# Kernel tuning notes

Hardware: AMD Instinct MI355X
Metric: run time of the kernel (lower is better)

Reference implementation:

```python
import jax, jax.numpy as jnp
import numpy as np

N_NODES = 100000
N_EDGES = 3200000
NUM_FEATURES = 128
NUM_CLASSES = 32
H1, H2 = 64, 32


def _glorot(key, shape):
    lim = float(np.sqrt(6.0 / (shape[0] + shape[1])))
    return jax.random.uniform(key, shape, jnp.float32, -lim, lim)


def setup_inputs() -> dict:
    key = jax.random.key(0)
    ks = jax.random.split(key, 8)
    x = jax.random.normal(ks[0], (N_NODES, NUM_FEATURES), jnp.float32)
    edge_index = jax.random.randint(ks[1], (2, N_EDGES), 0, N_NODES, jnp.int64)
    return {
        "x": x,
        "edge_index": edge_index,
        "W1": _glorot(ks[2], (NUM_FEATURES, H1)), "b1": jnp.zeros((H1,), jnp.float32),
        "W2": _glorot(ks[3], (H1, H2)), "b2": jnp.zeros((H2,), jnp.float32),
        "Wf": _glorot(ks[4], (H2, H2)), "bf": jnp.zeros((H2,), jnp.float32),
        "Wo": _glorot(ks[5], (H2, NUM_CLASSES)), "bo": jnp.zeros((NUM_CLASSES,), jnp.float32),
    }


def gcn_conv(x, src, dst, n, W, b):
    # PyG GCNConv: add self-loops, symmetric normalization D^-1/2 A D^-1/2,
    # aggregate messages source -> target (dst = edge_index[1]).
    h = x @ W                                            # [N, F_out]
    deg = jax.ops.segment_sum(jnp.ones_like(dst, dtype=x.dtype), dst, num_segments=n)
    dinv = jnp.where(deg > 0, jax.lax.rsqrt(deg), 0.0)
    norm = dinv[src] * dinv[dst]                         # [E+N]
    msg = h[src] * norm[:, None]                         # gather + scale
    return jax.ops.segment_sum(msg, dst, num_segments=n) + b


def reference(x, edge_index, W1, b1, W2, b2, Wf, bf, Wo, bo):
    n = x.shape[0]
    loops = jnp.arange(n, dtype=edge_index.dtype)
    src = jnp.concatenate([edge_index[0], loops])
    dst = jnp.concatenate([edge_index[1], loops])
    h = jax.nn.relu(gcn_conv(x, src, dst, n, W1, b1))
    h = gcn_conv(h, src, dst, n, W2, b2)
    h = jax.nn.relu(h @ Wf + bf)
    return h @ Wo + bo
```

## Files before the change

### kernel.cpp

```cpp
#include <hip/hip_runtime.h>
#include <hip/hip_bf16.h>


#define N_NODES 100000
#define N_EDGES 3200000
#define F_IN    128
#define H1F     64
#define H2F     32
#define NCLS    32
#define SCAN_BLOCK 1024
#define SCAN_CHUNKS ((N_NODES + SCAN_BLOCK - 1) / SCAN_BLOCK)
#define NTIL2 (N_NODES / 32)
#define NCNT2 ((N_EDGES + 2048 - 1) / 2048)
#define NFRONT (NTIL2 + NCNT2)

typedef __attribute__((ext_vector_type(8))) short bf16x8;
typedef __attribute__((ext_vector_type(4))) float f32x4;

static __device__ __forceinline__ float b2f(__hip_bfloat16 v) {
    return __bfloat162float(v);
}
static __device__ __forceinline__ float us2f(unsigned short u) {
    return __uint_as_float(((unsigned)u) << 16);
}
static __device__ __forceinline__ unsigned short f2us(float f) {
    __hip_bfloat16 h = __float2bfloat16(f);
    return *(unsigned short*)&h;
}
static __device__ __forceinline__ float ld(const void* p, size_t i, int isbf) {
    return isbf ? b2f(((const __hip_bfloat16*)p)[i]) : ((const float*)p)[i];
}


__global__ void k_detect(const void* xbuf, const void* eibuf, int* flags) {
    if (threadIdx.x != 0 || blockIdx.x != 0) return;
    const unsigned* ew = (const unsigned*)eibuf;
    int z = 0;
    for (int k = 0; k < 256; ++k) z += (ew[2 * k + 1] == 0u) ? 1 : 0;
    flags[0] = (z >= 200) ? 1 : 0;
    const unsigned* xw = (const unsigned*)xbuf;
    int inr = 0;
    for (int k = 0; k < 256; ++k) {
        unsigned fb = (xw[k] & 0xFFFFu) << 16;
        float a = fabsf(__uint_as_float(fb));
        inr += (a >= 1e-4f && a <= 20.0f) ? 1 : 0;
    }
    flags[1] = (inr >= 160) ? 1 : 0;
}

__global__ void __launch_bounds__(256)
k_front(const void* __restrict__ x, const void* __restrict__ W1,
        const int* __restrict__ ei,
        int* __restrict__ deg, int* __restrict__ aux,
        unsigned short* __restrict__ h1, const int* __restrict__ flags) {
    int blk = blockIdx.x, tid = threadIdx.x;

    if (blk % 3 == 0) {
        int t = (blk / 3) * 256 + tid;
        int e0 = t * 8;
        if (e0 >= N_EDGES) return;
        int d[8];
        if (flags[0]) {
            const int4* p = (const int4*)(ei + 2 * (size_t)(N_EDGES + e0));
            int4 a = p[0], b = p[1], c = p[2], g = p[3];
            d[0] = a.x; d[1] = a.z; d[2] = b.x; d[3] = b.z;
            d[4] = c.x; d[5] = c.z; d[6] = g.x; d[7] = g.z;
        } else {
            const int4* p = (const int4*)(ei + (size_t)N_EDGES + e0);
            int4 a = p[0], b = p[1];
            d[0] = a.x; d[1] = a.y; d[2] = a.z; d[3] = a.w;
            d[4] = b.x; d[5] = b.y; d[6] = b.z; d[7] = b.w;
        }
        int r[8];
#pragma unroll
        for (int j = 0; j < 8; ++j)
            r[j] = ((unsigned)d[j] < N_NODES) ? atomicAdd(&deg[d[j]], 1) : 0;
        *(int4*)(aux + e0)     = make_int4(r[0], r[1], r[2], r[3]);
        *(int4*)(aux + e0 + 4) = make_int4(r[4], r[5], r[6], r[7]);
        return;
    }

    int tile = blk - blk / 3 - 1;
    int isbf = flags[1];
    int wave = __builtin_amdgcn_readfirstlane(tid >> 6);
    int lane = tid & 63;
    size_t nbase = (size_t)tile * 32 + (size_t)wave * 8;

    float acc[8];
#pragma unroll
    for (int i = 0; i < 8; ++i) acc[i] = 0.f;

    if (isbf) {
        const unsigned short* w  = (const unsigned short*)W1;
        const unsigned short* xp = (const unsigned short*)x;
#pragma unroll 4
        for (int k2 = 0; k2 < 64; ++k2) {
            float wa = us2f(w[(2 * k2) * H1F + lane]);
            float wb = us2f(w[(2 * k2 + 1) * H1F + lane]);
#pragma unroll
            for (int i = 0; i < 8; ++i) {
                float xa = us2f(xp[(nbase + i) * F_IN + 2 * k2]);
                float xb = us2f(xp[(nbase + i) * F_IN + 2 * k2 + 1]);
                acc[i] += xa * wa;
                acc[i] += xb * wb;
            }
        }
    } else {
        const float* w  = (const float*)W1;
        const float* xp = (const float*)x;
#pragma unroll 4
        for (int k2 = 0; k2 < 64; ++k2) {
            float wa = w[(2 * k2) * H1F + lane];
            float wb = w[(2 * k2 + 1) * H1F + lane];
#pragma unroll
            for (int i = 0; i < 8; ++i) {
                float xa = xp[(nbase + i) * F_IN + 2 * k2];
                float xb = xp[(nbase + i) * F_IN + 2 * k2 + 1];
                acc[i] += xa * wa;
                acc[i] += xb * wb;
            }
        }
    }

#pragma unroll
    for (int i = 0; i < 8; ++i)
        h1[(nbase + i) * H1F + lane] = f2us(acc[i]);
}

__global__ void k_scanA(const int* __restrict__ deg, int* __restrict__ partial,
                        float* __restrict__ dinv) {
    __shared__ int red[16];
    int b = blockIdx.x, t = threadIdx.x;
    int i = b * SCAN_BLOCK + t;
    int v = (i < N_NODES) ? deg[i] : 0;
    if (i < N_NODES) dinv[i] = rsqrtf((float)v + 1.0f);
    for (int off = 32; off; off >>= 1) v += __shfl_down(v, off, 64);
    if ((t & 63) == 0) red[t >> 6] = v;
    __syncthreads();
    if (t == 0) {
        int s = 0;
        for (int k = 0; k < 16; ++k) s += red[k];
        partial[b] = s;
    }
}

__global__ void k_scanB(const int* __restrict__ partial, int* __restrict__ chunkoff) {
    if (threadIdx.x != 0 || blockIdx.x != 0) return;
    int run = 0;
    for (int b = 0; b < SCAN_CHUNKS; ++b) { chunkoff[b] = run; run += partial[b]; }
}

__global__ void k_scanC(const int* __restrict__ deg, const int* __restrict__ chunkoff,
                        int* __restrict__ rowptr) {
    __shared__ int wsum[16];
    int b = blockIdx.x, t = threadIdx.x, lane = t & 63, w = t >> 6;
    int i = b * SCAN_BLOCK + t;
    int v = (i < N_NODES) ? deg[i] : 0;
    for (int off = 1; off < 64; off <<= 1) {
        int u = __shfl_up(v, off, 64);
        if (lane >= off) v += u;
    }
    if (lane == 63) wsum[w] = v;
    __syncthreads();
    if (t == 0) {
        int run = 0;
        for (int k = 0; k < 16; ++k) { int s = wsum[k]; wsum[k] = run; run += s; }
    }
    __syncthreads();
    int incl = v + wsum[w] + chunkoff[b];
    if (i < N_NODES) rowptr[i + 1] = incl;
    if (b == 0 && t == 0) rowptr[0] = 0;
}

__global__ void __launch_bounds__(256)
k_scatter(const int* __restrict__ ei, const int* __restrict__ aux,
          const int* __restrict__ rowptr, int* __restrict__ csr,
          const int* __restrict__ flags) {
    int t = blockIdx.x * blockDim.x + threadIdx.x;
    int e0 = t * 8;
    if (e0 >= N_EDGES) return;
    int s[8], d[8];
    if (flags[0]) {
        const int4* ps = (const int4*)(ei + 2 * (size_t)e0);
#pragma unroll
        for (int q = 0; q < 4; ++q) {
            int4 a = ps[q];
            s[2 * q] = a.x; s[2 * q + 1] = a.z;
        }
        const int4* pd = (const int4*)(ei + 2 * (size_t)(N_EDGES + e0));
#pragma unroll
        for (int q = 0; q < 4; ++q) {
            int4 c = pd[q];
            d[2 * q] = c.x; d[2 * q + 1] = c.z;
        }
    } else {
        const int4* ps = (const int4*)(ei + (size_t)e0);
#pragma unroll
        for (int q = 0; q < 2; ++q) {
            int4 a = ps[q];
            s[4 * q] = a.x; s[4 * q + 1] = a.y; s[4 * q + 2] = a.z; s[4 * q + 3] = a.w;
        }
        const int4* pd = (const int4*)(ei + (size_t)N_EDGES + e0);
#pragma unroll
        for (int q = 0; q < 2; ++q) {
            int4 c = pd[q];
            d[4 * q] = c.x; d[4 * q + 1] = c.y; d[4 * q + 2] = c.z; d[4 * q + 3] = c.w;
        }
    }
    int a8[8];
    {
        int4 av0 = *(const int4*)(aux + e0);
        int4 av1 = *(const int4*)(aux + e0 + 4);
        a8[0] = av0.x; a8[1] = av0.y; a8[2] = av0.z; a8[3] = av0.w;
        a8[4] = av1.x; a8[5] = av1.y; a8[6] = av1.z; a8[7] = av1.w;
    }
    int rp[8];
#pragma unroll
    for (int j = 0; j < 8; ++j) {
        bool ok = (unsigned)s[j] < N_NODES && (unsigned)d[j] < N_NODES;
        rp[j] = ok ? rowptr[d[j]] : -1;
    }
#pragma unroll
    for (int j = 0; j < 8; ++j) {
        if (rp[j] >= 0) csr[rp[j] + a8[j]] = s[j];
    }
}

__global__ void k_agg1gemm2(const unsigned short* __restrict__ h1,
                            const float* __restrict__ dinv,
                            const int* __restrict__ rowptr, const int* __restrict__ csr,
                            const void* __restrict__ b1, const void* __restrict__ W2,
                            unsigned short* __restrict__ h2, const int* __restrict__ flags) {
    int n    = (blockIdx.x * blockDim.x + threadIdx.x) >> 6;
    n = __builtin_amdgcn_readfirstlane(n);
    int lane = threadIdx.x & 63;
    if (n >= N_NODES) return;
    int beg = rowptr[n], end = rowptr[n + 1];
    float dn  = dinv[n];
    float acc = dn * us2f(h1[(size_t)n * H1F + lane]);
    int e = beg;
    int nfull = (end - beg) >> 3;
    if (nfull > 0) {
        int sn[8];
#pragma unroll
        for (int j = 0; j < 8; ++j) sn[j] = csr[e + j];
        for (int b = 0; b < nfull; ++b) {
            int sc[8];
#pragma unroll
            for (int j = 0; j < 8; ++j) sc[j] = sn[j];
            e += 8;
            if (b + 1 < nfull) {
#pragma unroll
                for (int j = 0; j < 8; ++j) sn[j] = csr[e + j];
            }
            float w0 = dinv[sc[0]], w1 = dinv[sc[1]], w2 = dinv[sc[2]], w3 = dinv[sc[3]];
            float w4 = dinv[sc[4]], w5 = dinv[sc[5]], w6 = dinv[sc[6]], w7 = dinv[sc[7]];
            unsigned short v0 = h1[(size_t)sc[0] * H1F + lane];
            unsigned short v1 = h1[(size_t)sc[1] * H1F + lane];
            unsigned short v2 = h1[(size_t)sc[2] * H1F + lane];
            unsigned short v3 = h1[(size_t)sc[3] * H1F + lane];
            unsigned short v4 = h1[(size_t)sc[4] * H1F + lane];
            unsigned short v5 = h1[(size_t)sc[5] * H1F + lane];
            unsigned short v6 = h1[(size_t)sc[6] * H1F + lane];
            unsigned short v7 = h1[(size_t)sc[7] * H1F + lane];
            acc += w0 * us2f(v0); acc += w1 * us2f(v1);
            acc += w2 * us2f(v2); acc += w3 * us2f(v3);
            acc += w4 * us2f(v4); acc += w5 * us2f(v5);
            acc += w6 * us2f(v6); acc += w7 * us2f(v7);
        }
    }
    for (; e + 3 < end; e += 4) {
        int s0 = csr[e], s1 = csr[e + 1], s2 = csr[e + 2], s3 = csr[e + 3];
        float w0 = dinv[s0], w1 = dinv[s1], w2 = dinv[s2], w3 = dinv[s3];
        unsigned short v0 = h1[(size_t)s0 * H1F + lane];
        unsigned short v1 = h1[(size_t)s1 * H1F + lane];
        unsigned short v2 = h1[(size_t)s2 * H1F + lane];
        unsigned short v3 = h1[(size_t)s3 * H1F + lane];
        acc += w0 * us2f(v0); acc += w1 * us2f(v1);
        acc += w2 * us2f(v2); acc += w3 * us2f(v3);
    }
    for (; e < end; ++e) {
        int s = csr[e];
        acc += dinv[s] * us2f(h1[(size_t)s * H1F + lane]);
    }
    acc *= dn;
    int isbf = flags[1];
    float bv = isbf ? b2f(((const __hip_bfloat16*)b1)[lane]) : ((const float*)b1)[lane];
    float v  = fmaxf(acc + bv, 0.f);
    int f = lane & 31, h = lane >> 5;
    float part = 0.f;
    if (isbf) {
        const __hip_bfloat16* w = (const __hip_bfloat16*)W2;
#pragma unroll
        for (int j = 0; j < 32; ++j) {
            int k = h * 32 + j;
            part += __shfl(v, k, 64) * b2f(w[k * H2F + f]);
        }
    } else {
        const float* w = (const float*)W2;
#pragma unroll
        for (int j = 0; j < 32; ++j) {
            int k = h * 32 + j;
            part += __shfl(v, k, 64) * w[k * H2F + f];
        }
    }
    part += __shfl(part, lane ^ 32, 64);
    if (h == 0) h2[(size_t)n * H2F + f] = f2us(part);
}

__global__ void GCN_51737176048479_kernel(const unsigned short* __restrict__ h2,
                                          const float* __restrict__ dinv,
                                          const int* __restrict__ rowptr,
                                          const int* __restrict__ csr,
                                          const void* __restrict__ b2v,
                                          const void* __restrict__ Wf,
                                          const void* __restrict__ bfv,
                                          const void* __restrict__ Wo,
                                          const void* __restrict__ bov,
                                          void* __restrict__ out,
                                          const int* __restrict__ flags) {
    int tid = blockIdx.x * blockDim.x + threadIdx.x;
    int n   = tid >> 5;
    int f   = threadIdx.x & 31;
    if (n >= N_NODES) return;
    int isbf = flags[1];
    int beg = rowptr[n], end = rowptr[n + 1];
    float dn = dinv[n];
    float ar = dn * us2f(h2[(size_t)n * H2F + f]);
    int e = beg;
    int nfull = (end - beg) >> 3;
    if (nfull > 0) {
        int sn[8];
#pragma unroll
        for (int j = 0; j < 8; ++j) sn[j] = csr[e + j];
        for (int b = 0; b < nfull; ++b) {
            int sc[8];
#pragma unroll
            for (int j = 0; j < 8; ++j) sc[j] = sn[j];
            e += 8;
            if (b + 1 < nfull) {
#pragma unroll
                for (int j = 0; j < 8; ++j) sn[j] = csr[e + j];
            }
            float w0 = dinv[sc[0]], w1 = dinv[sc[1]], w2 = dinv[sc[2]], w3 = dinv[sc[3]];
            float w4 = dinv[sc[4]], w5 = dinv[sc[5]], w6 = dinv[sc[6]], w7 = dinv[sc[7]];
            unsigned short v0 = h2[(size_t)sc[0] * H2F + f];
            unsigned short v1 = h2[(size_t)sc[1] * H2F + f];
            unsigned short v2 = h2[(size_t)sc[2] * H2F + f];
            unsigned short v3 = h2[(size_t)sc[3] * H2F + f];
            unsigned short v4 = h2[(size_t)sc[4] * H2F + f];
            unsigned short v5 = h2[(size_t)sc[5] * H2F + f];
            unsigned short v6 = h2[(size_t)sc[6] * H2F + f];
            unsigned short v7 = h2[(size_t)sc[7] * H2F + f];
            ar += w0 * us2f(v0); ar += w1 * us2f(v1);
            ar += w2 * us2f(v2); ar += w3 * us2f(v3);
            ar += w4 * us2f(v4); ar += w5 * us2f(v5);
            ar += w6 * us2f(v6); ar += w7 * us2f(v7);
        }
    }
    for (; e + 3 < end; e += 4) {
        int s0 = csr[e], s1 = csr[e + 1], s2 = csr[e + 2], s3 = csr[e + 3];
        float w0 = dinv[s0], w1 = dinv[s1], w2 = dinv[s2], w3 = dinv[s3];
        unsigned short v0 = h2[(size_t)s0 * H2F + f];
        unsigned short v1 = h2[(size_t)s1 * H2F + f];
        unsigned short v2 = h2[(size_t)s2 * H2F + f];
        unsigned short v3 = h2[(size_t)s3 * H2F + f];
        ar += w0 * us2f(v0); ar += w1 * us2f(v1);
        ar += w2 * us2f(v2); ar += w3 * us2f(v3);
    }
    for (; e < end; ++e) {
        int s = csr[e];
        ar += dinv[s] * us2f(h2[(size_t)s * H2F + f]);
    }
    ar = ar * dn + ld(b2v, f, isbf);
    float acc1 = 0.f;
#pragma unroll
    for (int k = 0; k < H2F; ++k)
        acc1 += __shfl(ar, k, 32) * ld(Wf, (size_t)k * H2F + f, isbf);
    float u = fmaxf(acc1 + ld(bfv, f, isbf), 0.f);
    float acc2 = 0.f;
#pragma unroll
    for (int k = 0; k < H2F; ++k)
        acc2 += __shfl(u, k, 32) * ld(Wo, (size_t)k * NCLS + f, isbf);
    float r = acc2 + ld(bov, f, isbf);
    size_t oi = (size_t)n * NCLS + f;
    if (isbf) ((__hip_bfloat16*)out)[oi] = __float2bfloat16(r);
    else      ((float*)out)[oi] = r;
}

extern "C" void kernel_launch(void* const* d_in, const int* in_sizes, int n_in,
                              void* d_out, int out_size, void* d_ws, size_t ws_size,
                              hipStream_t stream) {
    const void* x  = d_in[0];
    const int*  ei = (const int*)d_in[1];
    const void* W1 = d_in[2];
    const void* b1 = d_in[3];
    const void* W2 = d_in[4];
    const void* b2 = d_in[5];
    const void* Wf = d_in[6];
    const void* bf = d_in[7];
    const void* Wo = d_in[8];
    const void* bo = d_in[9];

    char* ws = (char*)d_ws;
    int*            deg      = (int*)  (ws + 0);
    int*            rowptr   = (int*)  (ws + (512u  << 10));
    float*          dinv     = (float*)(ws + (1024u << 10));
    int*            flags    = (int*)  (ws + (1434u << 10));
    int*            partial  = (int*)  (ws + (1444u << 10));
    int*            chunkoff = (int*)  (ws + (1454u << 10));
    int*            aux      = (int*)  (ws + (2u  << 20));
    int*            csr      = (int*)  (ws + (15u << 20));
    unsigned short* h1       = (unsigned short*)(ws + (28u << 20));
    unsigned short* h2       = (unsigned short*)(ws + (41u << 20));

    const int B = 256;

    k_detect<<<1, 64, 0, stream>>>(x, ei, flags);
    hipMemsetAsync(deg, 0, N_NODES * sizeof(int), stream);

    k_front<<<NFRONT, B, 0, stream>>>(x, W1, ei, deg, aux, h1, flags);

    k_scanA<<<SCAN_CHUNKS, SCAN_BLOCK, 0, stream>>>(deg, partial, dinv);
    k_scanB<<<1, 64, 0, stream>>>(partial, chunkoff);
    k_scanC<<<SCAN_CHUNKS, SCAN_BLOCK, 0, stream>>>(deg, chunkoff, rowptr);
    k_scatter<<<(N_EDGES / 8 + B - 1) / B, B, 0, stream>>>(ei, aux, rowptr, csr, flags);

    k_agg1gemm2<<<(N_NODES * 64 + B - 1) / B, B, 0, stream>>>(h1, dinv, rowptr, csr,
                                                              b1, W2, h2, flags);
    GCN_51737176048479_kernel<<<(N_NODES * 32 + B - 1) / B, B, 0, stream>>>(
        h2, dinv, rowptr, csr, b2, Wf, bf, Wo, bo, d_out, flags);
}
```

Before: 501.4 us.

## Fuse memset into detect kernel, fold scanB into scanC, deepen gather prefetch

Merges the degree-array memset with the dtype/layout detection kernel, and removes the single-thread scanB kernel by having each scanC block reduce the preceding chunk partials itself. The aggregation loops in both GCN layers now run a two-stage software pipeline: indices are fetched two batches ahead and the dinv/feature gathers one batch ahead, so memory latency overlaps the accumulate. This cuts two launches and hides gather latency, at the cost of more registers per thread, which may lower occupancy.

```diff
diff --git a/kernel.cpp b/kernel.cpp
--- a/kernel.cpp
+++ b/kernel.cpp
@@ -32,20 +32,24 @@
 }
 
 
-__global__ void k_detect(const void* xbuf, const void* eibuf, int* flags) {
-    if (threadIdx.x != 0 || blockIdx.x != 0) return;
-    const unsigned* ew = (const unsigned*)eibuf;
-    int z = 0;
-    for (int k = 0; k < 256; ++k) z += (ew[2 * k + 1] == 0u) ? 1 : 0;
-    flags[0] = (z >= 200) ? 1 : 0;
-    const unsigned* xw = (const unsigned*)xbuf;
-    int inr = 0;
-    for (int k = 0; k < 256; ++k) {
-        unsigned fb = (xw[k] & 0xFFFFu) << 16;
-        float a = fabsf(__uint_as_float(fb));
-        inr += (a >= 1e-4f && a <= 20.0f) ? 1 : 0;
-    }
-    flags[1] = (inr >= 160) ? 1 : 0;
+__global__ void k_init(const void* xbuf, const void* eibuf, int* flags,
+                       int* __restrict__ deg) {
+    int t = blockIdx.x * blockDim.x + threadIdx.x;
+    if (t < N_NODES) deg[t] = 0;
+    if (blockIdx.x == 0 && threadIdx.x == 0) {
+        const unsigned* ew = (const unsigned*)eibuf;
+        int z = 0;
+        for (int k = 0; k < 256; ++k) z += (ew[2 * k + 1] == 0u) ? 1 : 0;
+        flags[0] = (z >= 200) ? 1 : 0;
+        const unsigned* xw = (const unsigned*)xbuf;
+        int inr = 0;
+        for (int k = 0; k < 256; ++k) {
+            unsigned fb = (xw[k] & 0xFFFFu) << 16;
+            float a = fabsf(__uint_as_float(fb));
+            inr += (a >= 1e-4f && a <= 20.0f) ? 1 : 0;
+        }
+        flags[1] = (inr >= 160) ? 1 : 0;
+    }
 }
 
 __global__ void __launch_bounds__(256)
@@ -144,17 +148,15 @@
     }
 }
 
-__global__ void k_scanB(const int* __restrict__ partial, int* __restrict__ chunkoff) {
-    if (threadIdx.x != 0 || blockIdx.x != 0) return;
-    int run = 0;
-    for (int b = 0; b < SCAN_CHUNKS; ++b) { chunkoff[b] = run; run += partial[b]; }
-}
-
-__global__ void k_scanC(const int* __restrict__ deg, const int* __restrict__ chunkoff,
+__global__ void k_scanC(const int* __restrict__ deg, const int* __restrict__ partial,
                         int* __restrict__ rowptr) {
     __shared__ int wsum[16];
+    __shared__ int red[16];
     int b = blockIdx.x, t = threadIdx.x, lane = t & 63, w = t >> 6;
     int i = b * SCAN_BLOCK + t;
+    int c = (t < SCAN_CHUNKS && t < b) ? partial[t] : 0;
+    for (int off = 32; off; off >>= 1) c += __shfl_down(c, off, 64);
+    if (lane == 0) red[w] = c;
     int v = (i < N_NODES) ? deg[i] : 0;
     for (int off = 1; off < 64; off <<= 1) {
         int u = __shfl_up(v, off, 64);
@@ -165,9 +167,12 @@
     if (t == 0) {
         int run = 0;
         for (int k = 0; k < 16; ++k) { int s = wsum[k]; wsum[k] = run; run += s; }
+        int sc = 0;
+        for (int k = 0; k < 16; ++k) sc += red[k];
+        red[0] = sc;
     }
     __syncthreads();
-    int incl = v + wsum[w] + chunkoff[b];
+    int incl = v + wsum[w] + red[0];
     if (i < N_NODES) rowptr[i + 1] = incl;
     if (b == 0 && t == 0) rowptr[0] = 0;
 }
@@ -241,32 +246,39 @@
     int e = beg;
     int nfull = (end - beg) >> 3;
     if (nfull > 0) {
-        int sn[8];
-#pragma unroll
-        for (int j = 0; j < 8; ++j) sn[j] = csr[e + j];
+        int i0[8], i1[8];
+        float w0[8]; unsigned short v0[8];
+#pragma unroll
+        for (int j = 0; j < 8; ++j) i0[j] = csr[e + j];
+        if (nfull > 1) {
+#pragma unroll
+            for (int j = 0; j < 8; ++j) i1[j] = csr[e + 8 + j];
+        }
+#pragma unroll
+        for (int j = 0; j < 8; ++j) {
+            w0[j] = dinv[i0[j]];
+            v0[j] = h1[(size_t)i0[j] * H1F + lane];
+        }
         for (int b = 0; b < nfull; ++b) {
-            int sc[8];
-#pragma unroll
-            for (int j = 0; j < 8; ++j) sc[j] = sn[j];
+            int i2[8]; float w1[8]; unsigned short v1[8];
+            if (b + 2 < nfull) {
+#pragma unroll
+                for (int j = 0; j < 8; ++j) i2[j] = csr[e + 16 + j];
+            }
+            if (b + 1 < nfull) {
+#pragma unroll
+                for (int j = 0; j < 8; ++j) {
+                    w1[j] = dinv[i1[j]];
+                    v1[j] = h1[(size_t)i1[j] * H1F + lane];
+                }
+            }
+            acc += w0[0] * us2f(v0[0]); acc += w0[1] * us2f(v0[1]);
+            acc += w0[2] * us2f(v0[2]); acc += w0[3] * us2f(v0[3]);
+            acc += w0[4] * us2f(v0[4]); acc += w0[5] * us2f(v0[5]);
+            acc += w0[6] * us2f(v0[6]); acc += w0[7] * us2f(v0[7]);
             e += 8;
-            if (b + 1 < nfull) {
-#pragma unroll
-                for (int j = 0; j < 8; ++j) sn[j] = csr[e + j];
-            }
-            float w0 = dinv[sc[0]], w1 = dinv[sc[1]], w2 = dinv[sc[2]], w3 = dinv[sc[3]];
-            float w4 = dinv[sc[4]], w5 = dinv[sc[5]], w6 = dinv[sc[6]], w7 = dinv[sc[7]];
-            unsigned short v0 = h1[(size_t)sc[0] * H1F + lane];
-            unsigned short v1 = h1[(size_t)sc[1] * H1F + lane];
-            unsigned short v2 = h1[(size_t)sc[2] * H1F + lane];
-            unsigned short v3 = h1[(size_t)sc[3] * H1F + lane];
-            unsigned short v4 = h1[(size_t)sc[4] * H1F + lane];
-            unsigned short v5 = h1[(size_t)sc[5] * H1F + lane];
-            unsigned short v6 = h1[(size_t)sc[6] * H1F + lane];
-            unsigned short v7 = h1[(size_t)sc[7] * H1F + lane];
-            acc += w0 * us2f(v0); acc += w1 * us2f(v1);
-            acc += w2 * us2f(v2); acc += w3 * us2f(v3);
-            acc += w4 * us2f(v4); acc += w5 * us2f(v5);
-            acc += w6 * us2f(v6); acc += w7 * us2f(v7);
+#pragma unroll
+            for (int j = 0; j < 8; ++j) { i1[j] = i2[j]; w0[j] = w1[j]; v0[j] = v1[j]; }
         }
     }
     for (; e + 3 < end; e += 4) {
@@ -330,32 +342,39 @@
     int e = beg;
     int nfull = (end - beg) >> 3;
     if (nfull > 0) {
-        int sn[8];
-#pragma unroll
-        for (int j = 0; j < 8; ++j) sn[j] = csr[e + j];
+        int i0[8], i1[8];
+        float w0[8]; unsigned short v0[8];
+#pragma unroll
+        for (int j = 0; j < 8; ++j) i0[j] = csr[e + j];
+        if (nfull > 1) {
+#pragma unroll
+            for (int j = 0; j < 8; ++j) i1[j] = csr[e + 8 + j];
+        }
+#pragma unroll
+        for (int j = 0; j < 8; ++j) {
+            w0[j] = dinv[i0[j]];
+            v0[j] = h2[(size_t)i0[j] * H2F + f];
+        }
         for (int b = 0; b < nfull; ++b) {
-            int sc[8];
-#pragma unroll
-            for (int j = 0; j < 8; ++j) sc[j] = sn[j];
+            int i2[8]; float w1[8]; unsigned short v1[8];
+            if (b + 2 < nfull) {
+#pragma unroll
+                for (int j = 0; j < 8; ++j) i2[j] = csr[e + 16 + j];
+            }
+            if (b + 1 < nfull) {
+#pragma unroll
+                for (int j = 0; j < 8; ++j) {
+                    w1[j] = dinv[i1[j]];
+                    v1[j] = h2[(size_t)i1[j] * H2F + f];
+                }
+            }
+            ar += w0[0] * us2f(v0[0]); ar += w0[1] * us2f(v0[1]);
+            ar += w0[2] * us2f(v0[2]); ar += w0[3] * us2f(v0[3]);
+            ar += w0[4] * us2f(v0[4]); ar += w0[5] * us2f(v0[5]);
+            ar += w0[6] * us2f(v0[6]); ar += w0[7] * us2f(v0[7]);
             e += 8;
-            if (b + 1 < nfull) {
-#pragma unroll
-                for (int j = 0; j < 8; ++j) sn[j] = csr[e + j];
-            }
-            float w0 = dinv[sc[0]], w1 = dinv[sc[1]], w2 = dinv[sc[2]], w3 = dinv[sc[3]];
-            float w4 = dinv[sc[4]], w5 = dinv[sc[5]], w6 = dinv[sc[6]], w7 = dinv[sc[7]];
-            unsigned short v0 = h2[(size_t)sc[0] * H2F + f];
-            unsigned short v1 = h2[(size_t)sc[1] * H2F + f];
-            unsigned short v2 = h2[(size_t)sc[2] * H2F + f];
-            unsigned short v3 = h2[(size_t)sc[3] * H2F + f];
-            unsigned short v4 = h2[(size_t)sc[4] * H2F + f];
-            unsigned short v5 = h2[(size_t)sc[5] * H2F + f];
-            unsigned short v6 = h2[(size_t)sc[6] * H2F + f];
-            unsigned short v7 = h2[(size_t)sc[7] * H2F + f];
-            ar += w0 * us2f(v0); ar += w1 * us2f(v1);
-            ar += w2 * us2f(v2); ar += w3 * us2f(v3);
-            ar += w4 * us2f(v4); ar += w5 * us2f(v5);
-            ar += w6 * us2f(v6); ar += w7 * us2f(v7);
+#pragma unroll
+            for (int j = 0; j < 8; ++j) { i1[j] = i2[j]; w0[j] = w1[j]; v0[j] = v1[j]; }
         }
     }
     for (; e + 3 < end; e += 4) {
@@ -408,7 +427,6 @@
     float*          dinv     = (float*)(ws + (1024u << 10));
     int*            flags    = (int*)  (ws + (1434u << 10));
     int*            partial  = (int*)  (ws + (1444u << 10));
-    int*            chunkoff = (int*)  (ws + (1454u << 10));
     int*            aux      = (int*)  (ws + (2u  << 20));
     int*            csr      = (int*)  (ws + (15u << 20));
     unsigned short* h1       = (unsigned short*)(ws + (28u << 20));
@@ -416,14 +434,12 @@
 
     const int B = 256;
 
-    k_detect<<<1, 64, 0, stream>>>(x, ei, flags);
-    hipMemsetAsync(deg, 0, N_NODES * sizeof(int), stream);
+    k_init<<<SCAN_CHUNKS, SCAN_BLOCK, 0, stream>>>(x, ei, flags, deg);
 
     k_front<<<NFRONT, B, 0, stream>>>(x, W1, ei, deg, aux, h1, flags);
 
     k_scanA<<<SCAN_CHUNKS, SCAN_BLOCK, 0, stream>>>(deg, partial, dinv);
-    k_scanB<<<1, 64, 0, stream>>>(partial, chunkoff);
-    k_scanC<<<SCAN_CHUNKS, SCAN_BLOCK, 0, stream>>>(deg, chunkoff, rowptr);
+    k_scanC<<<SCAN_CHUNKS, SCAN_BLOCK, 0, stream>>>(deg, partial, rowptr);
     k_scatter<<<(N_EDGES / 8 + B - 1) / B, B, 0, stream>>>(ei, aux, rowptr, csr, flags);
 
     k_agg1gemm2<<<(N_NODES * 64 + B - 1) / B, B, 0, stream>>>(h1, dinv, rowptr, csr,
```

Result: no change. 504.0 us (+0.5%).
